# Performance work log

Measured on AMD Instinct MI355X. Metric: run time of the kernel, lower is better.

## Reference

```python
import jax, jax.numpy as jnp
import numpy as np

N_NODES = 100000
N_EDGES = 1600000
IN_F, HID_F, OUT_F = 128, 128, 128


def setup_inputs() -> dict:
    key = jax.random.key(0)
    k1, k2, k3, k4, k5, k6 = jax.random.split(key, 6)
    x = jax.random.normal(k1, (N_NODES, IN_F), dtype=jnp.float32)
    edge_index = jax.random.randint(k2, (2, N_EDGES), 0, N_NODES, dtype=jnp.int32)
    # nn.Linear params (PyTorch layout: W [out, in], y = x @ W.T + b)
    s1 = 1.0 / np.sqrt(IN_F)
    W1 = jax.random.uniform(k3, (HID_F, IN_F), minval=-s1, maxval=s1, dtype=jnp.float32)
    b1 = jax.random.uniform(k4, (HID_F,), minval=-s1, maxval=s1, dtype=jnp.float32)
    s2 = 1.0 / np.sqrt(HID_F)
    W2 = jax.random.uniform(k5, (OUT_F, HID_F), minval=-s2, maxval=s2, dtype=jnp.float32)
    b2 = jax.random.uniform(k6, (OUT_F,), minval=-s2, maxval=s2, dtype=jnp.float32)
    return {"x": x, "edge_index": edge_index, "W1": W1, "b1": b1, "W2": W2, "b2": b2}


def _spmm_mean(h, row, col, deg_inv):
    # (adj @ h)[i] = sum_{edges e: row[e]==i} h[col[e]], then scale by deg_inv[i]
    agg = jax.ops.segment_sum(h[col], row, num_segments=N_NODES)
    return agg * deg_inv[:, None]


def reference(x, edge_index, W1, b1, W2, b2):
    row, col = edge_index[0], edge_index[1]
    # degree = row-sum of adjacency (duplicates in COO are summed, matching torch)
    deg = jax.ops.segment_sum(jnp.ones((N_EDGES,), dtype=x.dtype), row, num_segments=N_NODES)
    deg_inv = jnp.where(deg > 0, 1.0 / deg, 0.0)
    # dropout in eval mode = identity
    h = x @ W1.T + b1
    h = _spmm_mean(h, row, col, deg_inv)
    h = jax.nn.elu(h)
    h = h @ W2.T + b2
    h = _spmm_mean(h, row, col, deg_inv)
    return h
```

## Files before the change

kernel.cpp:

```cpp
#include <hip/hip_runtime.h>
#include <math.h>

#define N_NODES 100000
#define N_EDGES 1600000
#define F 128
#define NBUCK 196
#define EPB 4096
#define CAP 9216

typedef _Float16 f16x2 __attribute__((ext_vector_type(2)));
typedef _Float16 f16x8 __attribute__((ext_vector_type(8)));
typedef __fp16 fp16x2 __attribute__((ext_vector_type(2)));
typedef float f32x2 __attribute__((ext_vector_type(2)));
typedef float f32x4 __attribute__((ext_vector_type(4)));

__device__ inline uint pkrtz(float a, float b) {
    union { fp16x2 h; uint u; } c;
    c.h = __builtin_amdgcn_cvt_pkrtz(a, b);
    return c.u;
}
__device__ inline f16x2 as2(uint u) {
    union { uint u; f16x2 h; } c; c.u = u; return c.h;
}


__global__ __launch_bounds__(256) void bucketize_kernel(const int* __restrict__ row,
                                                        const int* __restrict__ col,
                                                        int* __restrict__ bucket_cursor,
                                                        int* __restrict__ pairs) {
    __shared__ int stage[EPB];
    __shared__ unsigned char bid[EPB];
    __shared__ int lcnt[NBUCK], lcur[NBUCK], loff[NBUCK], gbase[NBUCK];
    __shared__ int s[256];
    const int tid = threadIdx.x;
    const int base = blockIdx.x * EPB;
    const int cnt = min(N_EDGES - base, EPB);

    for (int i = tid; i < NBUCK; i += 256) { lcnt[i] = 0; lcur[i] = 0; }
    __syncthreads();
    for (int i = 0; i < EPB / 256; ++i) {
        int e = base + i * 256 + tid;
        if (e < N_EDGES) atomicAdd(&lcnt[row[e] >> 9], 1);
    }
    __syncthreads();
    {
        int v = (tid < NBUCK) ? lcnt[tid] : 0;
        s[tid] = v;
        __syncthreads();
        for (int off = 1; off < 256; off <<= 1) {
            int t = (tid >= off) ? s[tid - off] : 0;
            __syncthreads();
            s[tid] += t;
            __syncthreads();
        }
        if (tid < NBUCK) loff[tid] = s[tid] - v;
    }
    if (tid < NBUCK) {
        int c = lcnt[tid];
        gbase[tid] = c ? atomicAdd(&bucket_cursor[tid], c) : 0;
    }
    __syncthreads();
    for (int i = 0; i < EPB / 256; ++i) {
        int e = base + i * 256 + tid;
        if (e < N_EDGES) {
            int r = row[e], c = col[e];
            int b = r >> 9;
            int rk = atomicAdd(&lcur[b], 1);
            int q = loff[b] + rk;
            stage[q] = ((r & 511) << 17) | c;
            bid[q] = (unsigned char)b;
        }
    }
    __syncthreads();
    for (int q = tid; q < cnt; q += 256) {
        int b = bid[q];
        int t = gbase[b] + (q - loff[b]);
        if (t < CAP) pairs[b * CAP + t] = stage[q];
    }
}

__global__ __launch_bounds__(256) void bucket_scan_kernel(const int* __restrict__ bucket_cursor,
                                                          int* __restrict__ bucket_base) {
    __shared__ int s[256];
    const int tid = threadIdx.x;
    int v = (tid < NBUCK) ? bucket_cursor[tid] : 0;
    s[tid] = v;
    __syncthreads();
    for (int off = 1; off < 256; off <<= 1) {
        int t = (tid >= off) ? s[tid - off] : 0;
        __syncthreads();
        s[tid] += t;
        __syncthreads();
    }
    if (tid < NBUCK) bucket_base[tid] = s[tid] - v;
}

__global__ __launch_bounds__(512) void csr_finalize_kernel(const int* __restrict__ pairs,
                                                           const int* __restrict__ bucket_cursor,
                                                           const int* __restrict__ bucket_base,
                                                           int* __restrict__ csr_col,
                                                           int* __restrict__ row_start,
                                                           float* __restrict__ deg_inv) {
    __shared__ int rcnt[512], rcnt2[512], ssc[512], roff[512];
    __shared__ int colstage[CAP];
    const int tid = threadIdx.x;
    const int b = blockIdx.x;
    const int cnt = min(bucket_cursor[b], CAP);
    const int s0 = bucket_base[b];
    const int* reg = &pairs[b * CAP];

    rcnt[tid] = 0;
    rcnt2[tid] = 0;
    __syncthreads();
    for (int q = tid; q < cnt; q += 512) atomicAdd(&rcnt[reg[q] >> 17], 1);
    __syncthreads();
    const int d = rcnt[tid];
    ssc[tid] = d;
    __syncthreads();
    for (int off = 1; off < 512; off <<= 1) {
        int t = (tid >= off) ? ssc[tid - off] : 0;
        __syncthreads();
        ssc[tid] += t;
        __syncthreads();
    }
    const int excl = ssc[tid] - d;
    roff[tid] = excl;
    const int grow = (b << 9) + tid;
    if (grow < N_NODES) {
        row_start[grow] = s0 + excl;
        deg_inv[grow] = d ? 1.0f / (float)d : 0.0f;
    } else if (grow == N_NODES) {
        row_start[N_NODES] = s0 + excl;
    }
    __syncthreads();
    for (int q = tid; q < cnt; q += 512) {
        int v = reg[q];
        int lr = v >> 17;
        int rk = atomicAdd(&rcnt2[lr], 1);
        colstage[roff[lr] + rk] = v & 0x1FFFF;
    }
    __syncthreads();
    for (int q = tid; q < cnt; q += 512) csr_col[s0 + q] = colstage[q];
}


__global__ __launch_bounds__(256) void convert_w_kernel(const float* __restrict__ W1,
                                                        const float* __restrict__ W2,
                                                        uint* __restrict__ W1h,
                                                        uint* __restrict__ W2h) {
    int i = blockIdx.x * 256 + threadIdx.x;
    if (i < F * F / 2) {
        float2 a = *(const float2*)&W1[i * 2];
        float2 b = *(const float2*)&W2[i * 2];
        W1h[i] = pkrtz(a.x, a.y);
        W2h[i] = pkrtz(b.x, b.y);
    }
}


template <bool IN_F16>
__global__ __launch_bounds__(256, 4) void gemm_mfma_kernel(const void* __restrict__ Xv,
                                                           const ushort* __restrict__ Wh,
                                                           const float* __restrict__ bias,
                                                           ushort* __restrict__ Y) {
    __shared__ __align__(16) char smraw[4 * 16 * 132 * 4];
    ushort* xs = (ushort*)smraw;
    float (*ys)[16][132] = (float(*)[16][132])smraw;

    const int tid = threadIdx.x;
    const int m0 = blockIdx.x << 6;

    if (!IN_F16) {
        const float* X = (const float*)Xv;
        for (int i = 0; i < 8; ++i) {
            int f = i * 256 + tid;
            int r = f >> 5, c = f & 31;
            int gr = m0 + r; gr = gr < N_NODES ? gr : N_NODES - 1;
            float4 v = *(const float4*)&X[(size_t)gr * F + (c << 2)];
            uint2 o = {pkrtz(v.x, v.y), pkrtz(v.z, v.w)};
            *(uint2*)&xs[r * 136 + (c << 2)] = o;
        }
    } else {
        const ushort* X = (const ushort*)Xv;
        for (int i = 0; i < 4; ++i) {
            int f = i * 256 + tid;
            int r = f >> 4, c = f & 15;
            int gr = m0 + r; gr = gr < N_NODES ? gr : N_NODES - 1;
            uint4 v = *(const uint4*)&X[(size_t)gr * F + (c << 3)];
            *(uint4*)&xs[r * 136 + (c << 3)] = v;
        }
    }
    __syncthreads();

    const int w = tid >> 6;
    const int lane = tid & 63;
    const int q = lane >> 4;
    const int t = lane & 15;

    f16x8 afr[4];
#pragma unroll
    for (int kk = 0; kk < 4; ++kk)
        afr[kk] = *(const f16x8*)&xs[(w * 16 + t) * 136 + kk * 32 + q * 8];

    f32x4 acc[8];
#pragma unroll
    for (int j = 0; j < 8; ++j) acc[j] = (f32x4){0.f, 0.f, 0.f, 0.f};

#pragma unroll
    for (int j = 0; j < 8; ++j) {
        const ushort* wrow = &Wh[(j * 16 + t) * F + q * 8];
#pragma unroll
        for (int kk = 0; kk < 4; ++kk) {
            f16x8 bfr = *(const f16x8*)&wrow[kk * 32];
            acc[j] = __builtin_amdgcn_mfma_f32_16x16x32_f16(afr[kk], bfr, acc[j], 0, 0, 0);
        }
    }

    __syncthreads();

#pragma unroll
    for (int j = 0; j < 8; ++j) {
        float bb = bias[j * 16 + t];
#pragma unroll
        for (int r = 0; r < 4; ++r) ys[w][q * 4 + r][j * 16 + t] = acc[j][r] + bb;
    }

    for (int i = 0; i < 4; ++i) {
        int c = i * 64 + lane;
        int row = c >> 4, seg = c & 15;
        int gr = m0 + w * 16 + row;
        if (gr < N_NODES) {
            const float* src = &ys[w][row][seg * 8];
            float4 a = *(const float4*)src;
            float4 b = *(const float4*)(src + 4);
            uint4 o = {pkrtz(a.x, a.y), pkrtz(a.z, a.w), pkrtz(b.x, b.y), pkrtz(b.z, b.w)};
            *(uint4*)&Y[(size_t)gr * F + seg * 8] = o;
        }
    }
}


template <bool ELU, bool OUT_F32>
__global__ __launch_bounds__(256) void spmm_kernel(const ushort* __restrict__ H,
                                                   const int* __restrict__ row_start,
                                                   const int* __restrict__ csr_col,
                                                   const float* __restrict__ deg_inv,
                                                   void* __restrict__ out) {
    const int node = blockIdx.x * 16 + (threadIdx.x >> 4);
    const int fo = (threadIdx.x & 15) << 3;

    const int s = row_start[node];
    const int e = row_start[node + 1];

    f32x2 a[4];
#pragma unroll
    for (int i = 0; i < 4; ++i) a[i] = (f32x2){0.f, 0.f};

    int p = s;
    while (p + 3 < e) {
        int c0 = csr_col[p], c1 = csr_col[p + 1], c2 = csr_col[p + 2], c3 = csr_col[p + 3];
        uint4 v0 = *(const uint4*)&H[(size_t)c0 * F + fo];
        uint4 v1 = *(const uint4*)&H[(size_t)c1 * F + fo];
        uint4 v2 = *(const uint4*)&H[(size_t)c2 * F + fo];
        uint4 v3 = *(const uint4*)&H[(size_t)c3 * F + fo];
        f16x2 h0 = (as2(v0.x) + as2(v1.x)) + (as2(v2.x) + as2(v3.x));
        f16x2 h1 = (as2(v0.y) + as2(v1.y)) + (as2(v2.y) + as2(v3.y));
        f16x2 h2 = (as2(v0.z) + as2(v1.z)) + (as2(v2.z) + as2(v3.z));
        f16x2 h3 = (as2(v0.w) + as2(v1.w)) + (as2(v2.w) + as2(v3.w));
        a[0] += (f32x2){(float)h0.x, (float)h0.y};
        a[1] += (f32x2){(float)h1.x, (float)h1.y};
        a[2] += (f32x2){(float)h2.x, (float)h2.y};
        a[3] += (f32x2){(float)h3.x, (float)h3.y};
        p += 4;
    }
    if (p + 1 < e) {
        int c0 = csr_col[p], c1 = csr_col[p + 1];
        uint4 v0 = *(const uint4*)&H[(size_t)c0 * F + fo];
        uint4 v1 = *(const uint4*)&H[(size_t)c1 * F + fo];
        f16x2 h0 = as2(v0.x) + as2(v1.x);
        f16x2 h1 = as2(v0.y) + as2(v1.y);
        f16x2 h2 = as2(v0.z) + as2(v1.z);
        f16x2 h3 = as2(v0.w) + as2(v1.w);
        a[0] += (f32x2){(float)h0.x, (float)h0.y};
        a[1] += (f32x2){(float)h1.x, (float)h1.y};
        a[2] += (f32x2){(float)h2.x, (float)h2.y};
        a[3] += (f32x2){(float)h3.x, (float)h3.y};
        p += 2;
    }
    if (p < e) {
        int c = csr_col[p];
        uint4 v = *(const uint4*)&H[(size_t)c * F + fo];
        f16x2 h0 = as2(v.x), h1 = as2(v.y), h2 = as2(v.z), h3 = as2(v.w);
        a[0] += (f32x2){(float)h0.x, (float)h0.y};
        a[1] += (f32x2){(float)h1.x, (float)h1.y};
        a[2] += (f32x2){(float)h2.x, (float)h2.y};
        a[3] += (f32x2){(float)h3.x, (float)h3.y};
    }

    const float di = deg_inv[node];
    float r[8];
#pragma unroll
    for (int i = 0; i < 4; ++i) { r[2 * i] = a[i].x * di; r[2 * i + 1] = a[i].y * di; }
    if (ELU) {
#pragma unroll
        for (int i = 0; i < 8; ++i) r[i] = (r[i] > 0.f) ? r[i] : expm1f(r[i]);
    }
    if (OUT_F32) {
        float* of = &((float*)out)[(size_t)node * F + fo];
        *(float4*)of = (float4){r[0], r[1], r[2], r[3]};
        *(float4*)(of + 4) = (float4){r[4], r[5], r[6], r[7]};
    } else {
        uint4 o = {pkrtz(r[0], r[1]), pkrtz(r[2], r[3]), pkrtz(r[4], r[5]), pkrtz(r[6], r[7])};
        *(uint4*)&((ushort*)out)[(size_t)node * F + fo] = o;
    }
}


extern "C" void kernel_launch(void* const* d_in, const int* in_sizes, int n_in,
                              void* d_out, int out_size, void* d_ws, size_t ws_size,
                              hipStream_t stream) {
    const float* x  = (const float*)d_in[0];
    const int*   ei = (const int*)d_in[1];
    const float* W1 = (const float*)d_in[2];
    const float* b1 = (const float*)d_in[3];
    const float* W2 = (const float*)d_in[4];
    const float* b2 = (const float*)d_in[5];
    float* out = (float*)d_out;

    const int* row = ei;
    const int* col = ei + N_EDGES;

    ushort* bufA = (ushort*)d_ws;
    ushort* bufB = bufA + (size_t)N_NODES * F;
    int* csr_col = (int*)(bufB + (size_t)N_NODES * F);
    int* row_start = csr_col + N_EDGES;
    float* deg_inv = (float*)(row_start + N_NODES + 4);
    int* bucket_cursor = (int*)(deg_inv + N_NODES);
    int* bucket_base   = bucket_cursor + 256;
    uint* W1h = (uint*)(bucket_base + 256);
    uint* W2h = W1h + F * F / 2;
    int* pairs = (int*)bufA;

    (void)hipMemsetAsync(bucket_cursor, 0, NBUCK * sizeof(int), stream);
    bucketize_kernel<<<(N_EDGES + EPB - 1) / EPB, 256, 0, stream>>>(row, col, bucket_cursor, pairs);
    bucket_scan_kernel<<<1, 256, 0, stream>>>(bucket_cursor, bucket_base);
    csr_finalize_kernel<<<NBUCK, 512, 0, stream>>>(pairs, bucket_cursor, bucket_base,
                                                   csr_col, row_start, deg_inv);

    convert_w_kernel<<<32, 256, 0, stream>>>(W1, W2, W1h, W2h);

    const int gemm_blocks = (N_NODES + 63) / 64;
    gemm_mfma_kernel<false><<<gemm_blocks, 256, 0, stream>>>(x, (const ushort*)W1h, b1, bufA);
    spmm_kernel<true, false><<<N_NODES / 16, 256, 0, stream>>>(bufA, row_start, csr_col, deg_inv, bufB);
    gemm_mfma_kernel<true><<<gemm_blocks, 256, 0, stream>>>(bufB, (const ushort*)W2h, b2, bufA);
    spmm_kernel<false, true><<<N_NODES / 16, 256, 0, stream>>>(bufA, row_start, csr_col, deg_inv, out);
}
```

Before: 327.6 us.

## Drop bucket scan kernel via padded CSR and wave-shuffle scans

Replaces the shared-memory Hillis-Steele scans in the bucketize and CSR finalize kernels with wave-level shuffle scans plus a small cross-wave fixup. It also removes the separate single-block bucket scan kernel. The CSR is now laid out with fixed per-bucket capacity, and per-row (start, degree) pairs replace the row_start prefix array. The aim is to cut one launch and the many barriers in the scans. In exchange, csr_col grows to the padded bucket size and the spmm kernels read an int2 per node.

```diff
diff --git a/kernel.cpp b/kernel.cpp
--- a/kernel.cpp
+++ b/kernel.cpp
@@ -21,6 +21,15 @@
 }
 __device__ inline f16x2 as2(uint u) {
     union { uint u; f16x2 h; } c; c.u = u; return c.h;
+}
+
+__device__ inline int wave_incl_scan(int v, int lane) {
+#pragma unroll
+    for (int off = 1; off < 64; off <<= 1) {
+        int t = __shfl_up(v, off);
+        if (lane >= off) v += t;
+    }
+    return v;
 }
 
 
@@ -31,8 +40,10 @@
     __shared__ int stage[EPB];
     __shared__ unsigned char bid[EPB];
     __shared__ int lcnt[NBUCK], lcur[NBUCK], loff[NBUCK], gbase[NBUCK];
-    __shared__ int s[256];
+    __shared__ int wsum[4];
     const int tid = threadIdx.x;
+    const int lane = tid & 63;
+    const int wid = tid >> 6;
     const int base = blockIdx.x * EPB;
     const int cnt = min(N_EDGES - base, EPB);
 
@@ -45,15 +56,16 @@
     __syncthreads();
     {
         int v = (tid < NBUCK) ? lcnt[tid] : 0;
-        s[tid] = v;
+        int inc = wave_incl_scan(v, lane);
+        if (lane == 63) wsum[wid] = inc;
         __syncthreads();
-        for (int off = 1; off < 256; off <<= 1) {
-            int t = (tid >= off) ? s[tid - off] : 0;
-            __syncthreads();
-            s[tid] += t;
-            __syncthreads();
-        }
-        if (tid < NBUCK) loff[tid] = s[tid] - v;
+        if (tid == 0) {
+            int a = 0;
+#pragma unroll
+            for (int i = 0; i < 4; ++i) { int t = wsum[i]; wsum[i] = a; a += t; }
+        }
+        __syncthreads();
+        if (tid < NBUCK) loff[tid] = inc - v + wsum[wid];
     }
     if (tid < NBUCK) {
         int c = lcnt[tid];
@@ -79,35 +91,21 @@
     }
 }
 
-__global__ __launch_bounds__(256) void bucket_scan_kernel(const int* __restrict__ bucket_cursor,
-                                                          int* __restrict__ bucket_base) {
-    __shared__ int s[256];
-    const int tid = threadIdx.x;
-    int v = (tid < NBUCK) ? bucket_cursor[tid] : 0;
-    s[tid] = v;
-    __syncthreads();
-    for (int off = 1; off < 256; off <<= 1) {
-        int t = (tid >= off) ? s[tid - off] : 0;
-        __syncthreads();
-        s[tid] += t;
-        __syncthreads();
-    }
-    if (tid < NBUCK) bucket_base[tid] = s[tid] - v;
-}
-
 __global__ __launch_bounds__(512) void csr_finalize_kernel(const int* __restrict__ pairs,
                                                            const int* __restrict__ bucket_cursor,
-                                                           const int* __restrict__ bucket_base,
                                                            int* __restrict__ csr_col,
-                                                           int* __restrict__ row_start,
+                                                           int2* __restrict__ rs,
                                                            float* __restrict__ deg_inv) {
-    __shared__ int rcnt[512], rcnt2[512], ssc[512], roff[512];
+    __shared__ int rcnt[512], rcnt2[512], roff[512];
     __shared__ int colstage[CAP];
+    __shared__ int wsum[8];
     const int tid = threadIdx.x;
+    const int lane = tid & 63;
+    const int wid = tid >> 6;
     const int b = blockIdx.x;
     const int cnt = min(bucket_cursor[b], CAP);
-    const int s0 = bucket_base[b];
-    const int* reg = &pairs[b * CAP];
+    const int base = b * CAP;
+    const int* reg = &pairs[base];
 
     rcnt[tid] = 0;
     rcnt2[tid] = 0;
@@ -115,22 +113,21 @@
     for (int q = tid; q < cnt; q += 512) atomicAdd(&rcnt[reg[q] >> 17], 1);
     __syncthreads();
     const int d = rcnt[tid];
-    ssc[tid] = d;
-    __syncthreads();
-    for (int off = 1; off < 512; off <<= 1) {
-        int t = (tid >= off) ? ssc[tid - off] : 0;
-        __syncthreads();
-        ssc[tid] += t;
-        __syncthreads();
-    }
-    const int excl = ssc[tid] - d;
+    int inc = wave_incl_scan(d, lane);
+    if (lane == 63) wsum[wid] = inc;
+    __syncthreads();
+    if (tid == 0) {
+        int a = 0;
+#pragma unroll
+        for (int i = 0; i < 8; ++i) { int t = wsum[i]; wsum[i] = a; a += t; }
+    }
+    __syncthreads();
+    const int excl = inc - d + wsum[wid];
     roff[tid] = excl;
     const int grow = (b << 9) + tid;
     if (grow < N_NODES) {
-        row_start[grow] = s0 + excl;
+        rs[grow] = make_int2(base + excl, d);
         deg_inv[grow] = d ? 1.0f / (float)d : 0.0f;
-    } else if (grow == N_NODES) {
-        row_start[N_NODES] = s0 + excl;
     }
     __syncthreads();
     for (int q = tid; q < cnt; q += 512) {
@@ -140,7 +137,7 @@
         colstage[roff[lr] + rk] = v & 0x1FFFF;
     }
     __syncthreads();
-    for (int q = tid; q < cnt; q += 512) csr_col[s0 + q] = colstage[q];
+    for (int q = tid; q < cnt; q += 512) csr_col[base + q] = colstage[q];
 }
 
 
@@ -242,15 +239,16 @@
 
 template <bool ELU, bool OUT_F32>
 __global__ __launch_bounds__(256) void spmm_kernel(const ushort* __restrict__ H,
-                                                   const int* __restrict__ row_start,
+                                                   const int2* __restrict__ rs,
                                                    const int* __restrict__ csr_col,
                                                    const float* __restrict__ deg_inv,
                                                    void* __restrict__ out) {
     const int node = blockIdx.x * 16 + (threadIdx.x >> 4);
     const int fo = (threadIdx.x & 15) << 3;
 
-    const int s = row_start[node];
-    const int e = row_start[node + 1];
+    const int2 sd = rs[node];
+    const int s = sd.x;
+    const int e = s + sd.y;
 
     f32x2 a[4];
 #pragma unroll
@@ -333,25 +331,22 @@
     ushort* bufA = (ushort*)d_ws;
     ushort* bufB = bufA + (size_t)N_NODES * F;
     int* csr_col = (int*)(bufB + (size_t)N_NODES * F);
-    int* row_start = csr_col + N_EDGES;
-    float* deg_inv = (float*)(row_start + N_NODES + 4);
+    int2* rs = (int2*)(csr_col + NBUCK * CAP);
+    float* deg_inv = (float*)(rs + N_NODES + 4);
     int* bucket_cursor = (int*)(deg_inv + N_NODES);
-    int* bucket_base   = bucket_cursor + 256;
-    uint* W1h = (uint*)(bucket_base + 256);
+    uint* W1h = (uint*)(bucket_cursor + 256);
     uint* W2h = W1h + F * F / 2;
     int* pairs = (int*)bufA;
 
     (void)hipMemsetAsync(bucket_cursor, 0, NBUCK * sizeof(int), stream);
     bucketize_kernel<<<(N_EDGES + EPB - 1) / EPB, 256, 0, stream>>>(row, col, bucket_cursor, pairs);
-    bucket_scan_kernel<<<1, 256, 0, stream>>>(bucket_cursor, bucket_base);
-    csr_finalize_kernel<<<NBUCK, 512, 0, stream>>>(pairs, bucket_cursor, bucket_base,
-                                                   csr_col, row_start, deg_inv);
+    csr_finalize_kernel<<<NBUCK, 512, 0, stream>>>(pairs, bucket_cursor, csr_col, rs, deg_inv);
 
     convert_w_kernel<<<32, 256, 0, stream>>>(W1, W2, W1h, W2h);
 
     const int gemm_blocks = (N_NODES + 63) / 64;
     gemm_mfma_kernel<false><<<gemm_blocks, 256, 0, stream>>>(x, (const ushort*)W1h, b1, bufA);
-    spmm_kernel<true, false><<<N_NODES / 16, 256, 0, stream>>>(bufA, row_start, csr_col, deg_inv, bufB);
+    spmm_kernel<true, false><<<N_NODES / 16, 256, 0, stream>>>(bufA, rs, csr_col, deg_inv, bufB);
     gemm_mfma_kernel<true><<<gemm_blocks, 256, 0, stream>>>(bufB, (const ushort*)W2h, b2, bufA);
-    spmm_kernel<false, true><<<N_NODES / 16, 256, 0, stream>>>(bufA, row_start, csr_col, deg_inv, out);
-}
+    spmm_kernel<false, true><<<N_NODES / 16, 256, 0, stream>>>(bufA, rs, csr_col, deg_inv, out);
+}
```

Result: faster. 318.5 us (-2.8%).
